# Optimization experiments

Hardware: AMD Instinct MI355X
Metric: run time of the kernel (lower is better)

Reference implementation:

```python
import jax, jax.numpy as jnp
import numpy as np

E, D, DIM, H, DH, MLP = 8, 6, 512, 8, 64, 512
P, S, NC, B = 4, 32, 10, 128
PD = 3 * P * P          # patch_dim = 48
GRID = S // P           # 8
N = GRID * GRID + 1     # 65 tokens (64 patches + cls)


def setup_inputs() -> dict:
    key = jax.random.key(0)
    ks = iter(jax.random.split(key, 16))
    r = lambda *s: jax.random.normal(next(ks), s, jnp.float32) * 0.02
    z = lambda *s: jnp.zeros(s, jnp.float32)
    o = lambda *s: jnp.ones(s, jnp.float32)
    return dict(
        x=jax.random.normal(next(ks), (B, 3, S, S), jnp.float32),
        gate_w=r(E, 3 * S * S), gate_b=z(E),
        pln1_g=o(E, PD), pln1_b=z(E, PD),
        patch_w=r(E, PD, DIM), patch_b=z(E, DIM),
        pln2_g=o(E, DIM), pln2_b=z(E, DIM),
        cls_tok=r(E, DIM), pos_emb=r(E, N, DIM),
        aln_g=o(E, D, DIM), aln_b=z(E, D, DIM),
        qkv_w=r(E, D, DIM, 3 * H * DH),
        out_w=r(E, D, H * DH, DIM), out_b=z(E, D, DIM),
        fln_g=o(E, D, DIM), fln_b=z(E, D, DIM),
        ff1_w=r(E, D, DIM, MLP), ff1_b=z(E, D, MLP),
        ff2_w=r(E, D, MLP, DIM), ff2_b=z(E, D, DIM),
        final_g=o(E, DIM), final_b=z(E, DIM),
        head_w=r(E, DIM, NC), head_b=z(E, NC))


def _ln(x, g, b):
    m = x.mean(-1, keepdims=True)
    v = ((x - m) ** 2).mean(-1, keepdims=True)
    return (x - m) * jax.lax.rsqrt(v + 1e-5) * g + b


LAYER_KEYS = ('aln_g', 'aln_b', 'qkv_w', 'out_w', 'out_b',
              'fln_g', 'fln_b', 'ff1_w', 'ff1_b', 'ff2_w', 'ff2_b')


def _vit(x, p):
    # x: [B, 3, S, S]; p: per-expert param dict (no leading expert axis)
    Bx = x.shape[0]
    # rearrange 'b c (h p1) (w p2) -> b (h w) (p1 p2 c)'
    t = x.reshape(Bx, 3, GRID, P, GRID, P).transpose(0, 2, 4, 3, 5, 1)
    t = t.reshape(Bx, GRID * GRID, PD)
    t = _ln(t, p['pln1_g'], p['pln1_b'])
    t = t @ p['patch_w'] + p['patch_b']
    t = _ln(t, p['pln2_g'], p['pln2_b'])
    cls = jnp.broadcast_to(p['cls_tok'][None, None, :], (Bx, 1, DIM))
    t = jnp.concatenate([cls, t], axis=1) + p['pos_emb'][None]  # [B, N, DIM]

    def block(t, lp):
        g = _ln(t, lp['aln_g'], lp['aln_b'])
        qkv = g @ lp['qkv_w']                       # [B, N, 3*H*DH]
        q, k, v = jnp.split(qkv, 3, axis=-1)
        q = q.reshape(Bx, N, H, DH).transpose(0, 2, 1, 3)
        k = k.reshape(Bx, N, H, DH).transpose(0, 2, 1, 3)
        v = v.reshape(Bx, N, H, DH).transpose(0, 2, 1, 3)
        att = jax.nn.softmax(jnp.einsum('bhid,bhjd->bhij', q, k) * (DH ** -0.5), axis=-1)
        o = jnp.einsum('bhij,bhjd->bhid', att, v).transpose(0, 2, 1, 3).reshape(Bx, N, H * DH)
        t = t + o @ lp['out_w'] + lp['out_b']
        g = _ln(t, lp['fln_g'], lp['fln_b'])
        f = jax.nn.gelu(g @ lp['ff1_w'] + lp['ff1_b'], approximate=False) @ lp['ff2_w'] + lp['ff2_b']
        return t + f, None

    layer_p = {k: p[k] for k in LAYER_KEYS}  # each [D, ...]
    t, _ = jax.lax.scan(block, t, layer_p)
    t = _ln(t, p['final_g'], p['final_b'])
    return t[:, 0] @ p['head_w'] + p['head_b']   # [B, NC]


def _moe(x, params):
    Bx = x.shape[0]
    logits = x.reshape(Bx, -1) @ params['gate_w'].T + params['gate_b']  # [B, E]
    top1 = jnp.argmax(logits, axis=1)                                   # [B]
    expert_p = {k: v for k, v in params.items() if k not in ('gate_w', 'gate_b')}
    all_out = jax.vmap(lambda pp: _vit(x, pp))(expert_p)                # [E, B, NC]
    return all_out[top1, jnp.arange(Bx)]                                # [B, NC]


def reference(x, gate_w, gate_b, pln1_g, pln1_b, patch_w, patch_b, pln2_g, pln2_b,
              cls_tok, pos_emb, aln_g, aln_b, qkv_w, out_w, out_b,
              fln_g, fln_b, ff1_w, ff1_b, ff2_w, ff2_b, final_g, final_b,
              head_w, head_b):
    params = {k: v for k, v in locals().items() if k != 'x'}
    return _moe(x, params)
```

## Files before the change

kernel.cpp:

```cpp
#include <hip/hip_runtime.h>
#include <math.h>

#define EXPERTS 8
#define DEPTH 6
#define DIM 512
#define HEADS 8
#define NCLS 10
#define BATCH 128
#define PD 48
#define NTOK 65
#define NRT 73
#define NROWSP (NRT * 128)

typedef __attribute__((ext_vector_type(4))) float f32x4;
typedef __attribute__((ext_vector_type(8))) __bf16 bf16x8;
typedef unsigned short u16;

#define GLOAD_LDS16(gp, lp)                                                     \
    __builtin_amdgcn_global_load_lds(                                           \
        (const __attribute__((address_space(1))) void*)(gp),                    \
        (__attribute__((address_space(3))) void*)(lp), 16, 0, 0)

__device__ inline u16 f2bf(float f) {
    union { float f; unsigned u; } v; v.f = f;
    unsigned r = v.u + 0x7FFFu + ((v.u >> 16) & 1u);
    return (u16)(r >> 16);
}
__device__ inline float bf2f(u16 s) {
    union { unsigned u; float f; } v; v.u = ((unsigned)s) << 16;
    return v.f;
}

__global__ __launch_bounds__(256) void gate_k(const float* __restrict__ x,
                                              const float* __restrict__ gw,
                                              const float* __restrict__ gb,
                                              int* __restrict__ top1) {
    int b = blockIdx.x, tid = threadIdx.x;
    const float* xb = x + (size_t)b * 3072;
    float acc[EXPERTS];
#pragma unroll
    for (int e = 0; e < EXPERTS; ++e) acc[e] = 0.f;
    for (int i = tid; i < 3072; i += 256) {
        float xv = xb[i];
#pragma unroll
        for (int e = 0; e < EXPERTS; ++e)
            acc[e] = fmaf(xv, gw[(size_t)e * 3072 + i], acc[e]);
    }
    __shared__ float red[256];
    __shared__ float logits[EXPERTS];
    for (int e = 0; e < EXPERTS; ++e) {
        red[tid] = acc[e];
        __syncthreads();
        for (int s = 128; s > 0; s >>= 1) {
            if (tid < s) red[tid] += red[tid + s];
            __syncthreads();
        }
        if (tid == 0) logits[e] = red[0] + gb[e];
        __syncthreads();
    }
    if (tid == 0) {
        int best = 0;
        float bv = logits[0];
        for (int e = 1; e < EXPERTS; ++e)
            if (logits[e] > bv) { bv = logits[e]; best = e; }
        top1[b] = best;
    }
}

__global__ __launch_bounds__(128) void route3_k(const int* __restrict__ top1,
                                                int* __restrict__ prow,
                                                int* __restrict__ tile_e) {
    __shared__ int t1[BATCH];
    int tid = threadIdx.x;
    t1[tid] = top1[tid];
    __syncthreads();
    if (tid != 0) return;
    int row = 0, tile = 0;
    for (int e = 0; e < EXPERTS; ++e) {
        int ne = 0;
        for (int b = 0; b < BATCH; ++b)
            if (t1[b] == e) { prow[b] = row + ne * 65; ne++; }
        if (!ne) continue;
        int nt = (ne * 65 + 127) >> 7;
        for (int tt = 0; tt < nt; ++tt) tile_e[tile++] = e;
        row += nt << 7;
    }
    for (; tile < NRT; ++tile) tile_e[tile] = -1;
}

__global__ __launch_bounds__(256) void patch_k(const float* __restrict__ x,
                                               const float* __restrict__ pln1_g,
                                               const float* __restrict__ pln1_b,
                                               const float* __restrict__ patch_w,
                                               const float* __restrict__ patch_b,
                                               const float* __restrict__ pln2_g,
                                               const float* __restrict__ pln2_b,
                                               const float* __restrict__ cls_tok,
                                               const float* __restrict__ pos_emb,
                                               const int* __restrict__ top1,
                                               const int* __restrict__ prow,
                                               float* __restrict__ t) {
    int n = blockIdx.x, b = blockIdx.y, tid = threadIdx.x;
    int e = top1[b];
    float* trow = t + ((size_t)prow[b] + n) * DIM;
    const float* pe = pos_emb + ((size_t)e * NTOK + n) * DIM;

    if (n == 0) {
        for (int d = tid; d < DIM; d += 256)
            trow[d] = cls_tok[e * DIM + d] + pe[d];
        return;
    }
    int pi = n - 1, h = pi >> 3, w = pi & 7;
    __shared__ float pv[PD];
    __shared__ float red[256];
    if (tid < PD) {
        int p1 = tid / 12, rem = tid % 12, p2 = rem / 3, c = rem % 3;
        pv[tid] = x[((size_t)b * 3 + c) * 1024 + (h * 4 + p1) * 32 + (w * 4 + p2)];
    }
    __syncthreads();
    float m = 0.f, q = 0.f;
    for (int j = 0; j < PD; ++j) { float v = pv[j]; m += v; q += v * v; }
    m *= (1.f / PD);
    q = q * (1.f / PD) - m * m;
    float rs = rsqrtf(q + 1e-5f);
    __syncthreads();
    if (tid < PD)
        pv[tid] = (pv[tid] - m) * rs * pln1_g[e * PD + tid] + pln1_b[e * PD + tid];
    __syncthreads();

    float acc0 = patch_b[e * DIM + tid];
    float acc1 = patch_b[e * DIM + tid + 256];
    for (int j = 0; j < PD; ++j) {
        float v = pv[j];
        const float* wr = patch_w + ((size_t)e * PD + j) * DIM;
        acc0 = fmaf(v, wr[tid], acc0);
        acc1 = fmaf(v, wr[tid + 256], acc1);
    }
    red[tid] = acc0 + acc1;
    __syncthreads();
    for (int s = 128; s > 0; s >>= 1) {
        if (tid < s) red[tid] += red[tid + s];
        __syncthreads();
    }
    float S = red[0];
    __syncthreads();
    red[tid] = acc0 * acc0 + acc1 * acc1;
    __syncthreads();
    for (int s = 128; s > 0; s >>= 1) {
        if (tid < s) red[tid] += red[tid + s];
        __syncthreads();
    }
    float Q = red[0];
    float mean = S * (1.f / DIM);
    float var = Q * (1.f / DIM) - mean * mean;
    float rs2 = rsqrtf(var + 1e-5f);
    trow[tid]       = (acc0 - mean) * rs2 * pln2_g[e * DIM + tid]       + pln2_b[e * DIM + tid]       + pe[tid];
    trow[tid + 256] = (acc1 - mean) * rs2 * pln2_g[e * DIM + tid + 256] + pln2_b[e * DIM + tid + 256] + pe[tid + 256];
}

__global__ __launch_bounds__(256) void ln2_k(const float* __restrict__ src,
                                             u16* __restrict__ dst,
                                             const float* __restrict__ gbase,
                                             const float* __restrict__ bbase,
                                             const int* __restrict__ tile_e,
                                             int gestride) {
    int row = blockIdx.x * 4 + (threadIdx.x >> 6);
    int lane = threadIdx.x & 63;
    int e = tile_e[row >> 7];
    if (e < 0) return;
    const float* s = src + (size_t)row * 512;
    float4 a = *(const float4*)&s[lane * 4];
    float4 b = *(const float4*)&s[256 + lane * 4];
    float sum = a.x + a.y + a.z + a.w + b.x + b.y + b.z + b.w;
    float sq = a.x * a.x + a.y * a.y + a.z * a.z + a.w * a.w +
               b.x * b.x + b.y * b.y + b.z * b.z + b.w * b.w;
#pragma unroll
    for (int off = 32; off > 0; off >>= 1) {
        sum += __shfl_xor(sum, off);
        sq += __shfl_xor(sq, off);
    }
    float mean = sum * (1.f / DIM);
    float rs = rsqrtf(sq * (1.f / DIM) - mean * mean + 1e-5f);
    const float* g = gbase + (size_t)e * gestride;
    const float* bb = bbase + (size_t)e * gestride;
    float4 g0 = *(const float4*)&g[lane * 4];
    float4 g1 = *(const float4*)&g[256 + lane * 4];
    float4 b0 = *(const float4*)&bb[lane * 4];
    float4 b1 = *(const float4*)&bb[256 + lane * 4];
    int swz = (row & 7) << 3;
    u16 o[4];
    o[0] = f2bf((a.x - mean) * rs * g0.x + b0.x);
    o[1] = f2bf((a.y - mean) * rs * g0.y + b0.y);
    o[2] = f2bf((a.z - mean) * rs * g0.z + b0.z);
    o[3] = f2bf((a.w - mean) * rs * g0.w + b0.w);
    *(int2*)&dst[(size_t)row * 512 + ((lane * 4) ^ swz)] = *(int2*)o;
    o[0] = f2bf((b.x - mean) * rs * g1.x + b1.x);
    o[1] = f2bf((b.y - mean) * rs * g1.y + b1.y);
    o[2] = f2bf((b.z - mean) * rs * g1.z + b1.z);
    o[3] = f2bf((b.w - mean) * rs * g1.w + b1.w);
    *(int2*)&dst[(size_t)row * 512 + ((256 + lane * 4) ^ swz)] = *(int2*)o;
}

__global__ __launch_bounds__(256) void wconv_k(const float* __restrict__ src,
                                               u16* __restrict__ dst, int N) {
    __shared__ float tile[32][33];
    int n0 = blockIdx.x * 32, k0 = blockIdx.y * 32, m = blockIdx.z;
    const float* s = src + (size_t)m * 512 * N;
    u16* d = dst + (size_t)m * 512 * N;
    int r = threadIdx.x >> 5, c = threadIdx.x & 31;
#pragma unroll
    for (int i = 0; i < 4; ++i)
        tile[r + i * 8][c] = s[(size_t)(k0 + r + i * 8) * N + n0 + c];
    __syncthreads();
#pragma unroll
    for (int i = 0; i < 4; ++i) {
        int n = n0 + r + i * 8;
        d[(size_t)n * 512 + ((k0 + c) ^ ((n & 7) << 3))] = f2bf(tile[c][r + i * 8]);
    }
}

template <int N, int OP>
__global__ __launch_bounds__(256) void mgemm5_k(const u16* __restrict__ A,
                                                const u16* __restrict__ Wtbase,
                                                const float* __restrict__ Bbase,
                                                void* __restrict__ Cptr,
                                                const int* __restrict__ tile_e,
                                                int westride, int bestride) {
    constexpr int CT = N / 128;
    int orig = blockIdx.x, nwg = NRT * CT;
    int q = nwg >> 3, r8 = nwg & 7;
    int xcd = orig & 7, off = orig >> 3;
    int wg = (xcd < r8 ? xcd * (q + 1) : r8 * (q + 1) + (xcd - r8) * q) + off;
    int tile = wg / CT, ct = wg - tile * CT;
    int e = tile_e[tile];
    if (e < 0) return;
    int row0 = tile * 128, c0 = ct * 128;
    const u16* Wt = Wtbase + (size_t)e * westride;

    int tid = threadIdx.x;
    int lane = tid & 63, w = tid >> 6;
    int rl = lane & 15, kg = lane >> 4;
    int wr = w >> 1, wc = w & 1;

    __shared__ __align__(16) u16 As[128 * 64];
    __shared__ __align__(16) u16 Bs[128 * 64];

    f32x4 acc[4][4];
#pragma unroll
    for (int mt = 0; mt < 4; ++mt)
#pragma unroll
        for (int nt = 0; nt < 4; ++nt) acc[mt][nt] = (f32x4){0.f, 0.f, 0.f, 0.f};

    const u16* Ag = A + (size_t)(row0 + w * 32 + (lane >> 3)) * 512 + (lane & 7) * 8;
    const u16* Bg = Wt + (size_t)(c0 + w * 32 + (lane >> 3)) * 512 + (lane & 7) * 8;
    u16* Asw = As + w * 2048;
    u16* Bsw = Bs + w * 2048;

    int blk0 = (kg ^ (rl & 7)) * 8;
    int blk1 = ((4 + kg) ^ (rl & 7)) * 8;

    for (int k0 = 0; k0 < 512; k0 += 64) {
#pragma unroll
        for (int i = 0; i < 4; ++i) {
            GLOAD_LDS16(Ag + k0 + i * 8 * 512, Asw + i * 512);
            GLOAD_LDS16(Bg + k0 + i * 8 * 512, Bsw + i * 512);
        }
        __syncthreads();
#pragma unroll
        for (int ks = 0; ks < 2; ++ks) {
            int blk = ks ? blk1 : blk0;
            bf16x8 av[4], bv[4];
#pragma unroll
            for (int i = 0; i < 4; ++i) {
                av[i] = *(const bf16x8*)&As[(wr * 64 + i * 16 + rl) * 64 + blk];
                bv[i] = *(const bf16x8*)&Bs[(wc * 64 + i * 16 + rl) * 64 + blk];
            }
#pragma unroll
            for (int mt = 0; mt < 4; ++mt)
#pragma unroll
                for (int nt = 0; nt < 4; ++nt)
                    acc[mt][nt] = __builtin_amdgcn_mfma_f32_16x16x32_bf16(
                        av[mt], bv[nt], acc[mt][nt], 0, 0, 0);
        }
        __syncthreads();
    }

    int rh = lane >> 4;
#pragma unroll
    for (int mt = 0; mt < 4; ++mt)
#pragma unroll
        for (int nt = 0; nt < 4; ++nt)
#pragma unroll
            for (int rr = 0; rr < 4; ++rr) {
                size_t grow = row0 + wr * 64 + mt * 16 + rh * 4 + rr;
                int c = c0 + wc * 64 + nt * 16 + rl;
                float v = acc[mt][nt][rr];
                if (OP == 0) {
                    ((u16*)Cptr)[grow * N + c] = f2bf(v);
                } else if (OP == 1) {
                    ((float*)Cptr)[grow * 512 + c] += v + Bbase[(size_t)e * bestride + c];
                } else {
                    float vb = v + Bbase[(size_t)e * bestride + c];
                    float gl = vb * 0.5f * (1.f + erff(vb * 0.70710678118f));
                    ((u16*)Cptr)[grow * 512 + (c ^ (((int)grow & 7) << 3))] = f2bf(gl);
                }
            }
}

#define ATT_LDS (23040 / 2 + 8320 / 2 + 12288 / 2)
__global__ __launch_bounds__(256) void attn2_k(const u16* __restrict__ qkv,
                                               u16* __restrict__ o,
                                               const int* __restrict__ prow) {
    int h = blockIdx.x, b = blockIdx.y, tid = threadIdx.x;
    int pr = prow[b];
    __shared__ __align__(16) u16 smem[ATT_LDS];
    u16* Qs = smem;
    u16* Ks = smem + 80 * 72;
    u16* Ps = smem;
    u16* Vs = smem + 2 * 80 * 72;
    u16* Vt = Vs + 65 * 64;

    const u16* base = qkv + (size_t)pr * 1536 + h * 64;

    for (int idx = tid; idx < 640; idx += 256) {
        int r = idx >> 3, q = idx & 7;
        int4 vq = {0, 0, 0, 0}, vk = {0, 0, 0, 0};
        if (r < NTOK) {
            vq = *(const int4*)&base[(size_t)r * 1536 + q * 8];
            vk = *(const int4*)&base[(size_t)r * 1536 + 512 + q * 8];
        }
        *(int4*)&Qs[r * 72 + q * 8] = vq;
        *(int4*)&Ks[r * 72 + q * 8] = vk;
    }
    for (int idx = tid; idx < 520; idx += 256) {
        int r = idx >> 3, q = idx & 7;
        *(int4*)&Vs[r * 64 + q * 8] = *(const int4*)&base[(size_t)r * 1536 + 1024 + q * 8];
    }
    __syncthreads();

    int lane = tid & 63, w = tid >> 6;
    int rl = lane & 15, kg = lane >> 4, g = lane >> 4;

    f32x4 acc[2][5];
#pragma unroll
    for (int mi = 0; mi < 2; ++mi)
#pragma unroll
        for (int nt = 0; nt < 5; ++nt) acc[mi][nt] = (f32x4){0.f, 0.f, 0.f, 0.f};

#pragma unroll
    for (int mi = 0; mi < 2; ++mi) {
        if (mi == 1 && w != 0) continue;
        int mt = (mi == 0) ? w : 4;
        bf16x8 av0 = *(const bf16x8*)&Qs[(mt * 16 + rl) * 72 + kg * 8];
        bf16x8 av1 = *(const bf16x8*)&Qs[(mt * 16 + rl) * 72 + 32 + kg * 8];
#pragma unroll
        for (int nt = 0; nt < 5; ++nt) {
            bf16x8 bv0 = *(const bf16x8*)&Ks[(nt * 16 + rl) * 72 + kg * 8];
            bf16x8 bv1 = *(const bf16x8*)&Ks[(nt * 16 + rl) * 72 + 32 + kg * 8];
            acc[mi][nt] = __builtin_amdgcn_mfma_f32_16x16x32_bf16(av0, bv0, acc[mi][nt], 0, 0, 0);
            acc[mi][nt] = __builtin_amdgcn_mfma_f32_16x16x32_bf16(av1, bv1, acc[mi][nt], 0, 0, 0);
        }
    }

    for (int idx = tid; idx < 768; idx += 256) {
        int d = idx & 63, kq = idx >> 6;
        u16 tmp[8];
#pragma unroll
        for (int j = 0; j < 8; ++j) {
            int k = kq * 8 + j;
            tmp[j] = (k < NTOK) ? Vs[k * 64 + d] : (u16)0;
        }
        *(int4*)&Vt[d * 96 + kq * 8] = *(int4*)tmp;
    }

#pragma unroll
    for (int mi = 0; mi < 2; ++mi) {
        if (mi == 1 && w != 0) continue;
#pragma unroll
        for (int r = 0; r < 4; ++r) {
            float m = -3.0e38f;
#pragma unroll
            for (int nt = 0; nt < 5; ++nt) {
                float s = acc[mi][nt][r] * 0.125f;
                if (nt * 16 + rl >= NTOK) s = -3.0e38f;
                acc[mi][nt][r] = s;
                m = fmaxf(m, s);
            }
            m = fmaxf(m, __shfl_xor(m, 1));
            m = fmaxf(m, __shfl_xor(m, 2));
            m = fmaxf(m, __shfl_xor(m, 4));
            m = fmaxf(m, __shfl_xor(m, 8));
            float sum = 0.f;
#pragma unroll
            for (int nt = 0; nt < 5; ++nt) {
                float p = expf(acc[mi][nt][r] - m);
                acc[mi][nt][r] = p;
                sum += p;
            }
            sum += __shfl_xor(sum, 1);
            sum += __shfl_xor(sum, 2);
            sum += __shfl_xor(sum, 4);
            sum += __shfl_xor(sum, 8);
            float inv = 1.f / sum;
#pragma unroll
            for (int nt = 0; nt < 5; ++nt) acc[mi][nt][r] *= inv;
        }
    }
    __syncthreads();

#pragma unroll
    for (int mi = 0; mi < 2; ++mi) {
        if (mi == 1 && w != 0) continue;
        int mt = (mi == 0) ? w : 4;
#pragma unroll
        for (int nt = 0; nt < 5; ++nt)
#pragma unroll
            for (int r = 0; r < 4; ++r)
                Ps[(mt * 16 + g * 4 + r) * 96 + nt * 16 + rl] = f2bf(acc[mi][nt][r]);
    }
    for (int idx = tid; idx < 160; idx += 256) {
        int r = idx >> 1, hf = idx & 1;
        *(int4*)&Ps[r * 96 + 80 + hf * 8] = (int4){0, 0, 0, 0};
    }
    __syncthreads();

#pragma unroll
    for (int mi = 0; mi < 2; ++mi) {
        if (mi == 1 && w != 0) continue;
        int mt = (mi == 0) ? w : 4;
#pragma unroll
        for (int dt = 0; dt < 4; ++dt) {
            f32x4 oa = {0.f, 0.f, 0.f, 0.f};
#pragma unroll
            for (int s2 = 0; s2 < 3; ++s2) {
                bf16x8 av = *(const bf16x8*)&Ps[(mt * 16 + rl) * 96 + s2 * 32 + kg * 8];
                bf16x8 bv = *(const bf16x8*)&Vt[(dt * 16 + rl) * 96 + s2 * 32 + kg * 8];
                oa = __builtin_amdgcn_mfma_f32_16x16x32_bf16(av, bv, oa, 0, 0, 0);
            }
#pragma unroll
            for (int r = 0; r < 4; ++r) {
                int row = mt * 16 + g * 4 + r;
                if (row < NTOK) {
                    int grow = pr + row;
                    int c = h * 64 + dt * 16 + rl;
                    o[(size_t)grow * DIM + (c ^ ((grow & 7) << 3))] = f2bf(oa[r]);
                }
            }
        }
    }
}

__global__ __launch_bounds__(64) void final_k(const float* __restrict__ t,
                                              const float* __restrict__ fg,
                                              const float* __restrict__ fb,
                                              const float* __restrict__ hw,
                                              const float* __restrict__ hb,
                                              const int* __restrict__ top1,
                                              const int* __restrict__ prow,
                                              float* __restrict__ out) {
    int b = blockIdx.x, lane = threadIdx.x;
    int e = top1[b];
    const float* row = t + (size_t)prow[b] * DIM;
    float v[8], s = 0.f, q = 0.f;
#pragma unroll
    for (int ii = 0; ii < 8; ++ii) {
        v[ii] = row[ii * 64 + lane];
        s += v[ii];
        q += v[ii] * v[ii];
    }
    for (int off = 32; off > 0; off >>= 1) {
        s += __shfl_xor(s, off);
        q += __shfl_xor(q, off);
    }
    float mean = s * (1.f / DIM);
    float var = q * (1.f / DIM) - mean * mean;
    float rs = rsqrtf(var + 1e-5f);
    float nv[8];
#pragma unroll
    for (int ii = 0; ii < 8; ++ii) {
        int d = ii * 64 + lane;
        nv[ii] = (v[ii] - mean) * rs * fg[e * DIM + d] + fb[e * DIM + d];
    }
    for (int c = 0; c < NCLS; ++c) {
        float p = 0.f;
#pragma unroll
        for (int ii = 0; ii < 8; ++ii) {
            int d = ii * 64 + lane;
            p = fmaf(nv[ii], hw[(size_t)e * DIM * NCLS + d * NCLS + c], p);
        }
        for (int off = 32; off > 0; off >>= 1) p += __shfl_xor(p, off);
        if (lane == 0) out[b * NCLS + c] = p + hb[e * NCLS + c];
    }
}

extern "C" void kernel_launch(void* const* d_in, const int* in_sizes, int n_in,
                              void* d_out, int out_size, void* d_ws, size_t ws_size,
                              hipStream_t stream) {
    const float* x       = (const float*)d_in[0];
    const float* gate_w  = (const float*)d_in[1];
    const float* gate_b  = (const float*)d_in[2];
    const float* pln1_g  = (const float*)d_in[3];
    const float* pln1_b  = (const float*)d_in[4];
    const float* patch_w = (const float*)d_in[5];
    const float* patch_b = (const float*)d_in[6];
    const float* pln2_g  = (const float*)d_in[7];
    const float* pln2_b  = (const float*)d_in[8];
    const float* cls_tok = (const float*)d_in[9];
    const float* pos_emb = (const float*)d_in[10];
    const float* aln_g   = (const float*)d_in[11];
    const float* aln_b   = (const float*)d_in[12];
    const float* qkv_w   = (const float*)d_in[13];
    const float* out_w   = (const float*)d_in[14];
    const float* out_b   = (const float*)d_in[15];
    const float* fln_g   = (const float*)d_in[16];
    const float* fln_b   = (const float*)d_in[17];
    const float* ff1_w   = (const float*)d_in[18];
    const float* ff1_b   = (const float*)d_in[19];
    const float* ff2_w   = (const float*)d_in[20];
    const float* ff2_b   = (const float*)d_in[21];
    const float* final_g = (const float*)d_in[22];
    const float* final_b = (const float*)d_in[23];
    const float* head_w  = (const float*)d_in[24];
    const float* head_b  = (const float*)d_in[25];
    float* out = (float*)d_out;

    int* top1   = (int*)d_ws;
    int* prow   = top1 + 128;
    int* tile_e = prow + 128;
    float* t  = (float*)((char*)d_ws + 4096);
    u16* aln  = (u16*)(t + (size_t)NROWSP * DIM);
    u16* qb16 = aln + (size_t)NROWSP * DIM;
    u16* ao16 = qb16 + (size_t)NROWSP * 1536;
    u16* h16  = ao16 + (size_t)NROWSP * DIM;
    u16* wq_t = h16 + (size_t)NROWSP * DIM;
    u16* wo_t = wq_t + (size_t)48 * 1536 * 512;
    u16* w1_t = wo_t + (size_t)48 * 512 * 512;
    u16* w2_t = w1_t + (size_t)48 * 512 * 512;

    gate_k<<<BATCH, 256, 0, stream>>>(x, gate_w, gate_b, top1);
    route3_k<<<1, 128, 0, stream>>>(top1, prow, tile_e);
    patch_k<<<dim3(NTOK, BATCH), 256, 0, stream>>>(x, pln1_g, pln1_b, patch_w, patch_b,
                                                   pln2_g, pln2_b, cls_tok, pos_emb,
                                                   top1, prow, t);
    wconv_k<<<dim3(48, 16, 48), 256, 0, stream>>>(qkv_w, wq_t, 1536);
    wconv_k<<<dim3(16, 16, 48), 256, 0, stream>>>(out_w, wo_t, 512);
    wconv_k<<<dim3(16, 16, 48), 256, 0, stream>>>(ff1_w, w1_t, 512);
    wconv_k<<<dim3(16, 16, 48), 256, 0, stream>>>(ff2_w, w2_t, 512);

    for (int l = 0; l < DEPTH; ++l) {
        ln2_k<<<NROWSP / 4, 256, 0, stream>>>(t, aln, aln_g + l * DIM, aln_b + l * DIM,
                                              tile_e, DEPTH * DIM);
        mgemm5_k<1536, 0><<<NRT * 12, 256, 0, stream>>>(
            aln, wq_t + (size_t)l * 1536 * 512, nullptr, qb16, tile_e,
            DEPTH * 512 * 1536, 0);
        attn2_k<<<dim3(HEADS, BATCH), 256, 0, stream>>>(qb16, ao16, prow);
        mgemm5_k<512, 1><<<NRT * 4, 256, 0, stream>>>(
            ao16, wo_t + (size_t)l * 512 * 512, out_b + l * DIM, t, tile_e,
            DEPTH * 512 * 512, DEPTH * DIM);
        ln2_k<<<NROWSP / 4, 256, 0, stream>>>(t, aln, fln_g + l * DIM, fln_b + l * DIM,
                                              tile_e, DEPTH * DIM);
        mgemm5_k<512, 2><<<NRT * 4, 256, 0, stream>>>(
            aln, w1_t + (size_t)l * 512 * 512, ff1_b + l * DIM, h16, tile_e,
            DEPTH * 512 * 512, DEPTH * DIM);
        mgemm5_k<512, 1><<<NRT * 4, 256, 0, stream>>>(
            h16, w2_t + (size_t)l * 512 * 512, ff2_b + l * DIM, t, tile_e,
            DEPTH * 512 * 512, DEPTH * DIM);
    }
    final_k<<<BATCH, 64, 0, stream>>>(t, final_g, final_b, head_w, head_b, top1, prow, out);
}
```

Measured before the change: 882.8 us.

## Use 256-row expert padding, smaller M tiles for N=512 GEMMs, 5-wave attention, fused wconv

Expert row groups are now padded to 256 rows instead of 128, and the GEMM kernel is templated on M tile height. The three N=512 GEMMs use 64-row tiles to launch more workgroups, while the QKV GEMM keeps 128-row tiles. Attention uses 320 threads so each of the five 16-row query tiles gets its own wave, replacing the imbalanced 4-wave scheme. The three 512x512 weight conversions are merged into one launch. The coarser padding adds wasted rows, and the smaller tiles give less reuse of the weight tile.

```diff
diff --git a/kernel.cpp b/kernel.cpp
--- a/kernel.cpp
+++ b/kernel.cpp
@@ -9,8 +9,8 @@
 #define BATCH 128
 #define PD 48
 #define NTOK 65
-#define NRT 73
-#define NROWSP (NRT * 128)
+#define NRT256 40
+#define NROWSP (NRT256 * 256)
 
 typedef __attribute__((ext_vector_type(4))) float f32x4;
 typedef __attribute__((ext_vector_type(8))) __bf16 bf16x8;
@@ -25,10 +25,6 @@
     union { float f; unsigned u; } v; v.f = f;
     unsigned r = v.u + 0x7FFFu + ((v.u >> 16) & 1u);
     return (u16)(r >> 16);
-}
-__device__ inline float bf2f(u16 s) {
-    union { unsigned u; float f; } v; v.u = ((unsigned)s) << 16;
-    return v.f;
 }
 
 __global__ __launch_bounds__(256) void gate_k(const float* __restrict__ x,
@@ -81,11 +77,11 @@
         for (int b = 0; b < BATCH; ++b)
             if (t1[b] == e) { prow[b] = row + ne * 65; ne++; }
         if (!ne) continue;
-        int nt = (ne * 65 + 127) >> 7;
+        int nt = (ne * 65 + 255) >> 8;
         for (int tt = 0; tt < nt; ++tt) tile_e[tile++] = e;
-        row += nt << 7;
-    }
-    for (; tile < NRT; ++tile) tile_e[tile] = -1;
+        row += nt << 8;
+    }
+    for (; tile < NRT256; ++tile) tile_e[tile] = -1;
 }
 
 __global__ __launch_bounds__(256) void patch_k(const float* __restrict__ x,
@@ -166,7 +162,7 @@
                                              int gestride) {
     int row = blockIdx.x * 4 + (threadIdx.x >> 6);
     int lane = threadIdx.x & 63;
-    int e = tile_e[row >> 7];
+    int e = tile_e[row >> 8];
     if (e < 0) return;
     const float* s = src + (size_t)row * 512;
     float4 a = *(const float4*)&s[lane * 4];
@@ -201,13 +197,11 @@
     *(int2*)&dst[(size_t)row * 512 + ((256 + lane * 4) ^ swz)] = *(int2*)o;
 }
 
-__global__ __launch_bounds__(256) void wconv_k(const float* __restrict__ src,
-                                               u16* __restrict__ dst, int N) {
+__device__ inline void wconv_body(const float* __restrict__ s,
+                                  u16* __restrict__ d, int N,
+                                  int n0, int k0, int tid) {
     __shared__ float tile[32][33];
-    int n0 = blockIdx.x * 32, k0 = blockIdx.y * 32, m = blockIdx.z;
-    const float* s = src + (size_t)m * 512 * N;
-    u16* d = dst + (size_t)m * 512 * N;
-    int r = threadIdx.x >> 5, c = threadIdx.x & 31;
+    int r = tid >> 5, c = tid & 31;
 #pragma unroll
     for (int i = 0; i < 4; ++i)
         tile[r + i * 8][c] = s[(size_t)(k0 + r + i * 8) * N + n0 + c];
@@ -219,22 +213,43 @@
     }
 }
 
-template <int N, int OP>
-__global__ __launch_bounds__(256) void mgemm5_k(const u16* __restrict__ A,
-                                                const u16* __restrict__ Wtbase,
-                                                const float* __restrict__ Bbase,
-                                                void* __restrict__ Cptr,
-                                                const int* __restrict__ tile_e,
-                                                int westride, int bestride) {
+__global__ __launch_bounds__(256) void wconv_k(const float* __restrict__ src,
+                                               u16* __restrict__ dst, int N) {
+    wconv_body(src + (size_t)blockIdx.z * 512 * N, dst + (size_t)blockIdx.z * 512 * N,
+               N, blockIdx.x * 32, blockIdx.y * 32, threadIdx.x);
+}
+
+__global__ __launch_bounds__(256) void wconv3_k(const float* __restrict__ s0,
+                                                const float* __restrict__ s1,
+                                                const float* __restrict__ s2,
+                                                u16* __restrict__ d0,
+                                                u16* __restrict__ d1,
+                                                u16* __restrict__ d2) {
+    int z = blockIdx.z, which = z / 48, m = z % 48;
+    const float* s = (which == 0) ? s0 : (which == 1) ? s1 : s2;
+    u16* d = (which == 0) ? d0 : (which == 1) ? d1 : d2;
+    wconv_body(s + (size_t)m * 512 * 512, d + (size_t)m * 512 * 512,
+               512, blockIdx.x * 32, blockIdx.y * 32, threadIdx.x);
+}
+
+template <int N, int OP, int MW>
+__global__ __launch_bounds__(256) void mgemm_k(const u16* __restrict__ A,
+                                               const u16* __restrict__ Wtbase,
+                                               const float* __restrict__ Bbase,
+                                               void* __restrict__ Cptr,
+                                               const int* __restrict__ tile_e,
+                                               int westride, int bestride) {
+    constexpr int M = MW * 32;
     constexpr int CT = N / 128;
-    int orig = blockIdx.x, nwg = NRT * CT;
+    constexpr int MTILES = NROWSP / M;
+    int orig = blockIdx.x, nwg = MTILES * CT;
     int q = nwg >> 3, r8 = nwg & 7;
     int xcd = orig & 7, off = orig >> 3;
     int wg = (xcd < r8 ? xcd * (q + 1) : r8 * (q + 1) + (xcd - r8) * q) + off;
     int tile = wg / CT, ct = wg - tile * CT;
-    int e = tile_e[tile];
+    int e = tile_e[(tile * M) >> 8];
     if (e < 0) return;
-    int row0 = tile * 128, c0 = ct * 128;
+    int row0 = tile * M, c0 = ct * 128;
     const u16* Wt = Wtbase + (size_t)e * westride;
 
     int tid = threadIdx.x;
@@ -242,18 +257,18 @@
     int rl = lane & 15, kg = lane >> 4;
     int wr = w >> 1, wc = w & 1;
 
-    __shared__ __align__(16) u16 As[128 * 64];
+    __shared__ __align__(16) u16 As[M * 64];
     __shared__ __align__(16) u16 Bs[128 * 64];
 
-    f32x4 acc[4][4];
-#pragma unroll
-    for (int mt = 0; mt < 4; ++mt)
+    f32x4 acc[MW][4];
+#pragma unroll
+    for (int mt = 0; mt < MW; ++mt)
 #pragma unroll
         for (int nt = 0; nt < 4; ++nt) acc[mt][nt] = (f32x4){0.f, 0.f, 0.f, 0.f};
 
-    const u16* Ag = A + (size_t)(row0 + w * 32 + (lane >> 3)) * 512 + (lane & 7) * 8;
+    const u16* Ag = A + (size_t)(row0 + w * (M / 4) + (lane >> 3)) * 512 + (lane & 7) * 8;
     const u16* Bg = Wt + (size_t)(c0 + w * 32 + (lane >> 3)) * 512 + (lane & 7) * 8;
-    u16* Asw = As + w * 2048;
+    u16* Asw = As + w * (M / 4) * 64;
     u16* Bsw = Bs + w * 2048;
 
     int blk0 = (kg ^ (rl & 7)) * 8;
@@ -261,22 +276,24 @@
 
     for (int k0 = 0; k0 < 512; k0 += 64) {
 #pragma unroll
-        for (int i = 0; i < 4; ++i) {
+        for (int i = 0; i < M / 32; ++i)
             GLOAD_LDS16(Ag + k0 + i * 8 * 512, Asw + i * 512);
+#pragma unroll
+        for (int i = 0; i < 4; ++i)
             GLOAD_LDS16(Bg + k0 + i * 8 * 512, Bsw + i * 512);
-        }
         __syncthreads();
 #pragma unroll
         for (int ks = 0; ks < 2; ++ks) {
             int blk = ks ? blk1 : blk0;
-            bf16x8 av[4], bv[4];
-#pragma unroll
-            for (int i = 0; i < 4; ++i) {
-                av[i] = *(const bf16x8*)&As[(wr * 64 + i * 16 + rl) * 64 + blk];
+            bf16x8 av[MW], bv[4];
+#pragma unroll
+            for (int i = 0; i < MW; ++i)
+                av[i] = *(const bf16x8*)&As[(wr * (M / 2) + i * 16 + rl) * 64 + blk];
+#pragma unroll
+            for (int i = 0; i < 4; ++i)
                 bv[i] = *(const bf16x8*)&Bs[(wc * 64 + i * 16 + rl) * 64 + blk];
-            }
-#pragma unroll
-            for (int mt = 0; mt < 4; ++mt)
+#pragma unroll
+            for (int mt = 0; mt < MW; ++mt)
 #pragma unroll
                 for (int nt = 0; nt < 4; ++nt)
                     acc[mt][nt] = __builtin_amdgcn_mfma_f32_16x16x32_bf16(
@@ -287,12 +304,12 @@
 
     int rh = lane >> 4;
 #pragma unroll
-    for (int mt = 0; mt < 4; ++mt)
+    for (int mt = 0; mt < MW; ++mt)
 #pragma unroll
         for (int nt = 0; nt < 4; ++nt)
 #pragma unroll
             for (int rr = 0; rr < 4; ++rr) {
-                size_t grow = row0 + wr * 64 + mt * 16 + rh * 4 + rr;
+                size_t grow = row0 + wr * (M / 2) + mt * 16 + rh * 4 + rr;
                 int c = c0 + wc * 64 + nt * 16 + rl;
                 float v = acc[mt][nt][rr];
                 if (OP == 0) {
@@ -308,10 +325,10 @@
 }
 
 #define ATT_LDS (23040 / 2 + 8320 / 2 + 12288 / 2)
-__global__ __launch_bounds__(256) void attn2_k(const u16* __restrict__ qkv,
+__global__ __launch_bounds__(320) void attn3_k(const u16* __restrict__ qkv,
                                                u16* __restrict__ o,
                                                const int* __restrict__ prow) {
-    int h = blockIdx.x, b = blockIdx.y, tid = threadIdx.x;
+    int b = blockIdx.x & 127, h = blockIdx.x >> 7, tid = threadIdx.x;
     int pr = prow[b];
     __shared__ __align__(16) u16 smem[ATT_LDS];
     u16* Qs = smem;
@@ -322,7 +339,7 @@
 
     const u16* base = qkv + (size_t)pr * 1536 + h * 64;
 
-    for (int idx = tid; idx < 640; idx += 256) {
+    for (int idx = tid; idx < 640; idx += 320) {
         int r = idx >> 3, q = idx & 7;
         int4 vq = {0, 0, 0, 0}, vk = {0, 0, 0, 0};
         if (r < NTOK) {
@@ -332,37 +349,32 @@
         *(int4*)&Qs[r * 72 + q * 8] = vq;
         *(int4*)&Ks[r * 72 + q * 8] = vk;
     }
-    for (int idx = tid; idx < 520; idx += 256) {
+    for (int idx = tid; idx < 520; idx += 320) {
         int r = idx >> 3, q = idx & 7;
         *(int4*)&Vs[r * 64 + q * 8] = *(const int4*)&base[(size_t)r * 1536 + 1024 + q * 8];
     }
     __syncthreads();
 
-    int lane = tid & 63, w = tid >> 6;
+    int lane = tid & 63, mt = tid >> 6;
     int rl = lane & 15, kg = lane >> 4, g = lane >> 4;
 
-    f32x4 acc[2][5];
-#pragma unroll
-    for (int mi = 0; mi < 2; ++mi)
-#pragma unroll
-        for (int nt = 0; nt < 5; ++nt) acc[mi][nt] = (f32x4){0.f, 0.f, 0.f, 0.f};
-
-#pragma unroll
-    for (int mi = 0; mi < 2; ++mi) {
-        if (mi == 1 && w != 0) continue;
-        int mt = (mi == 0) ? w : 4;
+    f32x4 acc[5];
+#pragma unroll
+    for (int nt = 0; nt < 5; ++nt) acc[nt] = (f32x4){0.f, 0.f, 0.f, 0.f};
+
+    {
         bf16x8 av0 = *(const bf16x8*)&Qs[(mt * 16 + rl) * 72 + kg * 8];
         bf16x8 av1 = *(const bf16x8*)&Qs[(mt * 16 + rl) * 72 + 32 + kg * 8];
 #pragma unroll
         for (int nt = 0; nt < 5; ++nt) {
             bf16x8 bv0 = *(const bf16x8*)&Ks[(nt * 16 + rl) * 72 + kg * 8];
             bf16x8 bv1 = *(const bf16x8*)&Ks[(nt * 16 + rl) * 72 + 32 + kg * 8];
-            acc[mi][nt] = __builtin_amdgcn_mfma_f32_16x16x32_bf16(av0, bv0, acc[mi][nt], 0, 0, 0);
-            acc[mi][nt] = __builtin_amdgcn_mfma_f32_16x16x32_bf16(av1, bv1, acc[mi][nt], 0, 0, 0);
-        }
-    }
-
-    for (int idx = tid; idx < 768; idx += 256) {
+            acc[nt] = __builtin_amdgcn_mfma_f32_16x16x32_bf16(av0, bv0, acc[nt], 0, 0, 0);
+            acc[nt] = __builtin_amdgcn_mfma_f32_16x16x32_bf16(av1, bv1, acc[nt], 0, 0, 0);
+        }
+    }
+
+    for (int idx = tid; idx < 768; idx += 320) {
         int d = idx & 63, kq = idx >> 6;
         u16 tmp[8];
 #pragma unroll
@@ -374,77 +386,63 @@
     }
 
 #pragma unroll
-    for (int mi = 0; mi < 2; ++mi) {
-        if (mi == 1 && w != 0) continue;
-#pragma unroll
-        for (int r = 0; r < 4; ++r) {
-            float m = -3.0e38f;
-#pragma unroll
-            for (int nt = 0; nt < 5; ++nt) {
-                float s = acc[mi][nt][r] * 0.125f;
-                if (nt * 16 + rl >= NTOK) s = -3.0e38f;
-                acc[mi][nt][r] = s;
-                m = fmaxf(m, s);
-            }
-            m = fmaxf(m, __shfl_xor(m, 1));
-            m = fmaxf(m, __shfl_xor(m, 2));
-            m = fmaxf(m, __shfl_xor(m, 4));
-            m = fmaxf(m, __shfl_xor(m, 8));
-            float sum = 0.f;
-#pragma unroll
-            for (int nt = 0; nt < 5; ++nt) {
-                float p = expf(acc[mi][nt][r] - m);
-                acc[mi][nt][r] = p;
-                sum += p;
-            }
-            sum += __shfl_xor(sum, 1);
-            sum += __shfl_xor(sum, 2);
-            sum += __shfl_xor(sum, 4);
-            sum += __shfl_xor(sum, 8);
-            float inv = 1.f / sum;
-#pragma unroll
-            for (int nt = 0; nt < 5; ++nt) acc[mi][nt][r] *= inv;
-        }
-    }
-    __syncthreads();
-
-#pragma unroll
-    for (int mi = 0; mi < 2; ++mi) {
-        if (mi == 1 && w != 0) continue;
-        int mt = (mi == 0) ? w : 4;
-#pragma unroll
-        for (int nt = 0; nt < 5; ++nt)
-#pragma unroll
-            for (int r = 0; r < 4; ++r)
-                Ps[(mt * 16 + g * 4 + r) * 96 + nt * 16 + rl] = f2bf(acc[mi][nt][r]);
-    }
-    for (int idx = tid; idx < 160; idx += 256) {
+    for (int r = 0; r < 4; ++r) {
+        float m = -3.0e38f;
+#pragma unroll
+        for (int nt = 0; nt < 5; ++nt) {
+            float s = acc[nt][r] * 0.125f;
+            if (nt * 16 + rl >= NTOK) s = -3.0e38f;
+            acc[nt][r] = s;
+            m = fmaxf(m, s);
+        }
+        m = fmaxf(m, __shfl_xor(m, 1));
+        m = fmaxf(m, __shfl_xor(m, 2));
+        m = fmaxf(m, __shfl_xor(m, 4));
+        m = fmaxf(m, __shfl_xor(m, 8));
+        float sum = 0.f;
+#pragma unroll
+        for (int nt = 0; nt < 5; ++nt) {
+            float p = expf(acc[nt][r] - m);
+            acc[nt][r] = p;
+            sum += p;
+        }
+        sum += __shfl_xor(sum, 1);
+        sum += __shfl_xor(sum, 2);
+        sum += __shfl_xor(sum, 4);
+        sum += __shfl_xor(sum, 8);
+        float inv = 1.f / sum;
+#pragma unroll
+        for (int nt = 0; nt < 5; ++nt) acc[nt][r] *= inv;
+    }
+    __syncthreads();
+
+#pragma unroll
+    for (int nt = 0; nt < 5; ++nt)
+#pragma unroll
+        for (int r = 0; r < 4; ++r)
+            Ps[(mt * 16 + g * 4 + r) * 96 + nt * 16 + rl] = f2bf(acc[nt][r]);
+    for (int idx = tid; idx < 160; idx += 320) {
         int r = idx >> 1, hf = idx & 1;
         *(int4*)&Ps[r * 96 + 80 + hf * 8] = (int4){0, 0, 0, 0};
     }
     __syncthreads();
 
 #pragma unroll
-    for (int mi = 0; mi < 2; ++mi) {
-        if (mi == 1 && w != 0) continue;
-        int mt = (mi == 0) ? w : 4;
-#pragma unroll
-        for (int dt = 0; dt < 4; ++dt) {
-            f32x4 oa = {0.f, 0.f, 0.f, 0.f};
-#pragma unroll
-            for (int s2 = 0; s2 < 3; ++s2) {
-                bf16x8 av = *(const bf16x8*)&Ps[(mt * 16 + rl) * 96 + s2 * 32 + kg * 8];
-                bf16x8 bv = *(const bf16x8*)&Vt[(dt * 16 + rl) * 96 + s2 * 32 + kg * 8];
-                oa = __builtin_amdgcn_mfma_f32_16x16x32_bf16(av, bv, oa, 0, 0, 0);
-            }
-#pragma unroll
-            for (int r = 0; r < 4; ++r) {
-                int row = mt * 16 + g * 4 + r;
-                if (row < NTOK) {
-                    int grow = pr + row;
-                    int c = h * 64 + dt * 16 + rl;
-                    o[(size_t)grow * DIM + (c ^ ((grow & 7) << 3))] = f2bf(oa[r]);
-                }
+    for (int dt = 0; dt < 4; ++dt) {
+        f32x4 oa = {0.f, 0.f, 0.f, 0.f};
+#pragma unroll
+        for (int s2 = 0; s2 < 3; ++s2) {
+            bf16x8 av = *(const bf16x8*)&Ps[(mt * 16 + rl) * 96 + s2 * 32 + kg * 8];
+            bf16x8 bv = *(const bf16x8*)&Vt[(dt * 16 + rl) * 96 + s2 * 32 + kg * 8];
+            oa = __builtin_amdgcn_mfma_f32_16x16x32_bf16(av, bv, oa, 0, 0, 0);
+        }
+#pragma unroll
+        for (int r = 0; r < 4; ++r) {
+            int row = mt * 16 + g * 4 + r;
+            if (row < NTOK) {
+                int grow = pr + row;
+                int c = h * 64 + dt * 16 + rl;
+                o[(size_t)grow * DIM + (c ^ ((grow & 7) << 3))] = f2bf(oa[r]);
             }
         }
     }
@@ -543,26 +541,24 @@
                                                    pln2_g, pln2_b, cls_tok, pos_emb,
                                                    top1, prow, t);
     wconv_k<<<dim3(48, 16, 48), 256, 0, stream>>>(qkv_w, wq_t, 1536);
-    wconv_k<<<dim3(16, 16, 48), 256, 0, stream>>>(out_w, wo_t, 512);
-    wconv_k<<<dim3(16, 16, 48), 256, 0, stream>>>(ff1_w, w1_t, 512);
-    wconv_k<<<dim3(16, 16, 48), 256, 0, stream>>>(ff2_w, w2_t, 512);
+    wconv3_k<<<dim3(16, 16, 144), 256, 0, stream>>>(out_w, ff1_w, ff2_w, wo_t, w1_t, w2_t);
 
     for (int l = 0; l < DEPTH; ++l) {
         ln2_k<<<NROWSP / 4, 256, 0, stream>>>(t, aln, aln_g + l * DIM, aln_b + l * DIM,
                                               tile_e, DEPTH * DIM);
-        mgemm5_k<1536, 0><<<NRT * 12, 256, 0, stream>>>(
+        mgemm_k<1536, 0, 4><<<(NROWSP / 128) * 12, 256, 0, stream>>>(
             aln, wq_t + (size_t)l * 1536 * 512, nullptr, qb16, tile_e,
             DEPTH * 512 * 1536, 0);
-        attn2_k<<<dim3(HEADS, BATCH), 256, 0, stream>>>(qb16, ao16, prow);
-        mgemm5_k<512, 1><<<NRT * 4, 256, 0, stream>>>(
+        attn3_k<<<HEADS * BATCH, 320, 0, stream>>>(qb16, ao16, prow);
+        mgemm_k<512, 1, 2><<<(NROWSP / 64) * 4, 256, 0, stream>>>(
             ao16, wo_t + (size_t)l * 512 * 512, out_b + l * DIM, t, tile_e,
             DEPTH * 512 * 512, DEPTH * DIM);
         ln2_k<<<NROWSP / 4, 256, 0, stream>>>(t, aln, fln_g + l * DIM, fln_b + l * DIM,
                                               tile_e, DEPTH * DIM);
-        mgemm5_k<512, 2><<<NRT * 4, 256, 0, stream>>>(
+        mgemm_k<512, 2, 2><<<(NROWSP / 64) * 4, 256, 0, stream>>>(
             aln, w1_t + (size_t)l * 512 * 512, ff1_b + l * DIM, h16, tile_e,
             DEPTH * 512 * 512, DEPTH * DIM);
-        mgemm5_k<512, 1><<<NRT * 4, 256, 0, stream>>>(
+        mgemm_k<512, 1, 2><<<(NROWSP / 64) * 4, 256, 0, stream>>>(
             h16, w2_t + (size_t)l * 512 * 512, ff2_b + l * DIM, t, tile_e,
             DEPTH * 512 * 512, DEPTH * DIM);
     }
```

Result: faster. 812.6 us (-8.0%).
